# Kernel optimization log

Measured on AMD Instinct MI355X. Metric: run time of the kernel, lower is better.

The kernel has to match this reference:

```python
import jax, jax.numpy as jnp
import numpy as np

DT = 0.1  # discretization step (matches init kwarg dt)


def setup_inputs() -> dict:
    key = jax.random.key(0)
    k1, k2, k3, k4 = jax.random.split(key, 4)
    Bsz, L, D, N = 16, 4096, 128, 64
    x = jax.random.normal(k1, (Bsz, L, D), dtype=jnp.float32)
    # torch uses torch.rand for A; shift by -N*I so A is Hurwitz and the
    # 4096-step recurrence stays numerically stable (same math, stable init).
    A = jax.random.uniform(k2, (D, N, N), dtype=jnp.float32) - float(N) * jnp.eye(N, dtype=jnp.float32)
    B = jax.random.uniform(k3, (D, N, 1), dtype=jnp.float32)
    C = jax.random.uniform(k4, (D, 1, N), dtype=jnp.float32)
    return {"x": x, "A": A, "B": B, "C": C}


def _discretize(A, B):
    # Bilinear (Tustin) transform, per channel d: [D, N, N]
    N = A.shape[-1]
    I = jnp.eye(N, dtype=A.dtype)[None, :, :]
    inv = jnp.linalg.inv(I - A * (DT / 2))
    A_bar = inv @ (I + A * (DT / 2))          # [D, N, N]
    B_bar = (inv @ B) * DT                    # [D, N, 1]
    return A_bar, B_bar


def reference(x, A, B, C):
    # x: [Bsz, L, D]; A: [D, N, N]; B: [D, N, 1]; C: [D, 1, N]
    Bsz, L, D = x.shape
    N = A.shape[-1]
    A_bar, B_bar = _discretize(A, B)
    Bb = B_bar[:, :, 0]                       # [D, N]
    Cv = C[:, 0, :]                           # [D, N]
    xs = jnp.moveaxis(x, 1, 0)                # [L, Bsz, D]
    h0 = jnp.zeros((Bsz, D, N), dtype=x.dtype)

    def step(h, x_t):
        # h_new[b,d,m] = sum_n A_bar[d,m,n] h[b,d,n] + x_t[b,d] * Bb[d,m]
        h = jnp.einsum('dmn,bdn->bdm', A_bar, h) + x_t[:, :, None] * Bb[None]
        y_t = jnp.einsum('bdn,dn->bd', h, Cv)
        return h, y_t

    _, ys = jax.lax.scan(step, h0, xs)        # ys: [L, Bsz, D]
    return jnp.moveaxis(ys, 0, 1)             # [Bsz, L, D]
```

## Files before the change

kernel.cpp:

```cpp
#include <hip/hip_runtime.h>

typedef float f4 __attribute__((ext_vector_type(4)));

#define PAD 68

#define SEED_C2 0.0251681f
#define SEED_C1 (-0.262380f)
#define SEED_C0 0.895613f

__device__ __forceinline__ void mm_acc(const float* L, const float* R,
                                       int i0, int j0, float acc[16]) {
  #pragma unroll
  for (int m = 0; m < 16; ++m) acc[m] = 0.f;
  #pragma unroll
  for (int n = 0; n < 64; n += 4) {
    f4 La[4], Rb[4];
    #pragma unroll
    for (int m = 0; m < 4; ++m) La[m] = *(const f4*)&L[(i0 + m) * PAD + n];
    #pragma unroll
    for (int p = 0; p < 4; ++p) Rb[p] = *(const f4*)&R[(n + p) * PAD + j0];
    #pragma unroll
    for (int m = 0; m < 4; ++m)
      #pragma unroll
      for (int p = 0; p < 4; ++p)
        #pragma unroll
        for (int c = 0; c < 4; ++c)
          acc[m * 4 + c] += La[m][p] * Rb[p][c];
  }
}

__device__ __forceinline__ void store_tile(float* Dst, int i0, int j0, const float acc[16]) {
  #pragma unroll
  for (int m = 0; m < 4; ++m) {
    f4 t = {acc[m*4+0], acc[m*4+1], acc[m*4+2], acc[m*4+3]};
    *(f4*)&Dst[(i0 + m) * PAD + j0] = t;
  }
}

__global__ __launch_bounds__(256) void s4_discretize(
    const float* __restrict__ Ag,
    const float* __restrict__ Bg,
    const float* __restrict__ Cg,
    float* __restrict__ Kout)
{
  __shared__ float Ms[64 * PAD];
  __shared__ float Xs[64 * PAD];
  __shared__ float Ts[64 * PAD];
  __shared__ float C4[4][65];
  __shared__ float U8[64][8];
  __shared__ float Bv[64], Cv0[64], Bb[64];
  __shared__ float Pr[4][64];

  const int d   = blockIdx.x;
  const int tid = threadIdx.x;
  const int i0  = (tid >> 4) << 2;
  const int j0  = (tid & 15) << 2;
  const int q   = tid >> 6;
  const int ln  = tid & 63;

  for (int idx = tid; idx < 4096; idx += 256) {
    int i = idx >> 6, j = idx & 63;
    float a = Ag[(size_t)d * 4096 + idx];
    Ms[i * PAD + j] = ((i == j) ? 1.f : 0.f) - 0.05f * a;
  }
  if (tid < 64) { Bv[tid] = Bg[d * 64 + tid]; Cv0[tid] = Cg[d * 64 + tid]; }
  __syncthreads();

  float acc[16];

  mm_acc(Ms, Ms, i0, j0, acc);
  store_tile(Ts, i0, j0, acc);
  __syncthreads();

  for (int idx = tid; idx < 4096; idx += 256) {
    int i = idx >> 6, j = idx & 63;
    Xs[i * PAD + j] = SEED_C2 * Ts[i * PAD + j] + SEED_C1 * Ms[i * PAD + j]
                    + ((i == j) ? SEED_C0 : 0.f);
  }
  __syncthreads();

  mm_acc(Ms, Xs, i0, j0, acc);
  store_tile(Ts, i0, j0, acc);
  __syncthreads();
  mm_acc(Xs, Ts, i0, j0, acc);
  __syncthreads();
  #pragma unroll
  for (int m = 0; m < 4; ++m) {
    f4 xo = *(const f4*)&Xs[(i0 + m) * PAD + j0];
    f4 t = {acc[m*4+0], acc[m*4+1], acc[m*4+2], acc[m*4+3]};
    *(f4*)&Xs[(i0 + m) * PAD + j0] = 2.f * xo - t;
  }
  __syncthreads();

  {
    float p = 0.f;
    #pragma unroll
    for (int m = 0; m < 16; ++m) p += Xs[ln * PAD + q * 16 + m] * Bv[q * 16 + m];
    Pr[q][ln] = p;
  }
  for (int idx = tid; idx < 4096; idx += 256) {
    int i = idx >> 6, j = idx & 63;
    Ms[i * PAD + j] = 2.f * Xs[i * PAD + j] - ((i == j) ? 1.f : 0.f);
  }
  __syncthreads();
  if (tid < 64) Bb[tid] = 0.1f * (Pr[0][tid] + Pr[1][tid] + Pr[2][tid] + Pr[3][tid]);
  __syncthreads();

  if (tid < 64) C4[0][tid] = Cv0[tid];
  __syncthreads();
  for (int j = 1; j < 4; ++j) {
    float p = 0.f;
    #pragma unroll
    for (int m = 0; m < 16; ++m) p += C4[j - 1][q * 16 + m] * Ms[(q * 16 + m) * PAD + ln];
    Pr[q][ln] = p;
    __syncthreads();
    if (q == 0) C4[j][ln] = Pr[0][ln] + Pr[1][ln] + Pr[2][ln] + Pr[3][ln];
    __syncthreads();
  }

  mm_acc(Ms, Ms, i0, j0, acc);
  #pragma unroll
  for (int m = 0; m < 4; ++m) {
    f4 t = {acc[m*4+0], acc[m*4+1], acc[m*4+2], acc[m*4+3]};
    *(f4*)&Ts[(i0 + m) * PAD + j0] = t;
  }
  __syncthreads();
  mm_acc(Ts, Ts, i0, j0, acc);
  __syncthreads();
  #pragma unroll
  for (int m = 0; m < 4; ++m) {
    f4 t = {acc[m*4+0], acc[m*4+1], acc[m*4+2], acc[m*4+3]};
    *(f4*)&Xs[(i0 + m) * PAD + j0] = t;
  }
  __syncthreads();

  if (tid < 64) U8[tid][0] = Bb[tid];
  __syncthreads();
  for (int i = 1; i < 8; ++i) {
    float p = 0.f;
    #pragma unroll
    for (int m = 0; m < 16; ++m) p += Xs[ln * PAD + q * 16 + m] * U8[q * 16 + m][i - 1];
    Pr[q][ln] = p;
    __syncthreads();
    if (q == 0) U8[ln][i] = Pr[0][ln] + Pr[1][ln] + Pr[2][ln] + Pr[3][ln];
    __syncthreads();
  }

  if (tid < 32) {
    int i = tid >> 2, j = tid & 3;
    float s = 0.f;
    #pragma unroll
    for (int n = 0; n < 64; ++n) s += C4[j][n] * U8[n][i];
    Kout[tid * 128 + d] = s;
  }
}

__global__ __launch_bounds__(256, 4) void s4_conv(
    const float* __restrict__ xg,
    const float* __restrict__ Ktg,
    float* __restrict__ yg)
{
  __shared__ float xs[287 * 32];
  __shared__ float Ks[32 * 32];

  const int tid = threadIdx.y * 32 + threadIdx.x;
  const int tc  = blockIdx.x;
  const int dq  = blockIdx.y;
  const int b   = blockIdx.z;
  const int d0  = dq * 32;
  const int t0  = tc * 256;

  for (int idx = tid; idx < 1024; idx += 256)
    Ks[idx] = Ktg[(idx >> 5) * 128 + d0 + (idx & 31)];

  const float* xb = xg + (size_t)b * 4096 * 128 + d0;
  for (int idx = tid; idx < 287 * 8; idx += 256) {
    int row = idx >> 3, c4 = (idx & 7) << 2;
    int t = t0 - 31 + row;
    f4 v = {0.f, 0.f, 0.f, 0.f};
    if (t >= 0) v = *(const f4*)&xb[(size_t)t * 128 + c4];
    *(f4*)&xs[row * 32 + c4] = v;
  }
  __syncthreads();

  const int dl = threadIdx.x;
  const int g  = threadIdx.y;

  float acc[32];
  #pragma unroll
  for (int t = 0; t < 32; ++t) acc[t] = 0.f;

  float w[47];
  #pragma unroll
  for (int k0 = 0; k0 < 32; k0 += 16) {
    const int base = g * 32 + 16 - k0;
    #pragma unroll
    for (int jj = 0; jj < 47; ++jj) w[jj] = xs[(base + jj) * 32 + dl];
    #pragma unroll
    for (int k = k0; k < k0 + 16; ++k) {
      float kv = Ks[k * 32 + dl];
      #pragma unroll
      for (int t = 0; t < 32; ++t)
        acc[t] += kv * w[t + (k0 + 15 - k)];
    }
  }

  float* yb = yg + ((size_t)b * 4096 + t0 + g * 32) * 128 + d0 + dl;
  #pragma unroll
  for (int t = 0; t < 32; ++t)
    yb[(size_t)t * 128] = acc[t];
}

extern "C" void kernel_launch(void* const* d_in, const int* in_sizes, int n_in,
                              void* d_out, int out_size, void* d_ws, size_t ws_size,
                              hipStream_t stream) {
  const float* x = (const float*)d_in[0];
  const float* A = (const float*)d_in[1];
  const float* B = (const float*)d_in[2];
  const float* C = (const float*)d_in[3];
  float* y  = (float*)d_out;
  float* Kt = (float*)d_ws;

  s4_discretize<<<128, 256, 0, stream>>>(A, B, C, Kt);
  dim3 grid(16, 4, 16), block(32, 8);
  s4_conv<<<grid, block, 0, stream>>>(x, Kt, y);
}
```

Before: 109.8 us.

## Restructure discretize kernel: fewer matmuls, 8x4 tiles, shuffle reductions

Reworks the per-channel discretization kernel. The seed computation is fused into the first matmul epilogue, and the Newton step now writes (2I - M·X) directly. The A_bar^4 squaring matmul is replaced by 15 sequential matrix-vector products with A_bar^2, combined with C and C·A_bar to form the 32 kernel taps. Matmuls use 8x4 register tiles on 128 threads, and the partial-sum reductions go through shared memory plus warp shuffles instead of a separate reduction pass. This cuts matmul count and barriers, but half the threads sit idle during matmuls and the matvec chain is longer; the conv kernel, which likely dominates runtime, is unchanged.

```diff
diff --git a/kernel.cpp b/kernel.cpp
--- a/kernel.cpp
+++ b/kernel.cpp
@@ -8,32 +8,24 @@
 #define SEED_C1 (-0.262380f)
 #define SEED_C0 0.895613f
 
-__device__ __forceinline__ void mm_acc(const float* L, const float* R,
-                                       int i0, int j0, float acc[16]) {
-  #pragma unroll
-  for (int m = 0; m < 16; ++m) acc[m] = 0.f;
+__device__ __forceinline__ void mm_acc8x4(const float* L, const float* R,
+                                          int i0, int j0, float acc[32]) {
+  #pragma unroll
+  for (int m = 0; m < 32; ++m) acc[m] = 0.f;
   #pragma unroll
   for (int n = 0; n < 64; n += 4) {
-    f4 La[4], Rb[4];
-    #pragma unroll
-    for (int m = 0; m < 4; ++m) La[m] = *(const f4*)&L[(i0 + m) * PAD + n];
+    f4 La[8], Rb[4];
+    #pragma unroll
+    for (int m = 0; m < 8; ++m) La[m] = *(const f4*)&L[(i0 + m) * PAD + n];
     #pragma unroll
     for (int p = 0; p < 4; ++p) Rb[p] = *(const f4*)&R[(n + p) * PAD + j0];
     #pragma unroll
-    for (int m = 0; m < 4; ++m)
+    for (int m = 0; m < 8; ++m)
       #pragma unroll
       for (int p = 0; p < 4; ++p)
         #pragma unroll
         for (int c = 0; c < 4; ++c)
           acc[m * 4 + c] += La[m][p] * Rb[p][c];
-  }
-}
-
-__device__ __forceinline__ void store_tile(float* Dst, int i0, int j0, const float acc[16]) {
-  #pragma unroll
-  for (int m = 0; m < 4; ++m) {
-    f4 t = {acc[m*4+0], acc[m*4+1], acc[m*4+2], acc[m*4+3]};
-    *(f4*)&Dst[(i0 + m) * PAD + j0] = t;
   }
 }
 
@@ -46,17 +38,18 @@
   __shared__ float Ms[64 * PAD];
   __shared__ float Xs[64 * PAD];
   __shared__ float Ts[64 * PAD];
-  __shared__ float C4[4][65];
-  __shared__ float U8[64][8];
-  __shared__ float Bv[64], Cv0[64], Bb[64];
+  __shared__ float U16[16][PAD];
   __shared__ float Pr[4][64];
+  __shared__ float Bv[64], Cv0[64], Bb[64], Cc1[64];
 
   const int d   = blockIdx.x;
   const int tid = threadIdx.x;
-  const int i0  = (tid >> 4) << 2;
+  const int i0  = (tid >> 4) << 3;
   const int j0  = (tid & 15) << 2;
   const int q   = tid >> 6;
   const int ln  = tid & 63;
+  const int co  = tid >> 2;
+  const int cc  = tid & 3;
 
   for (int idx = tid; idx < 4096; idx += 256) {
     int i = idx >> 6, j = idx & 63;
@@ -66,29 +59,44 @@
   if (tid < 64) { Bv[tid] = Bg[d * 64 + tid]; Cv0[tid] = Cg[d * 64 + tid]; }
   __syncthreads();
 
-  float acc[16];
-
-  mm_acc(Ms, Ms, i0, j0, acc);
-  store_tile(Ts, i0, j0, acc);
-  __syncthreads();
-
-  for (int idx = tid; idx < 4096; idx += 256) {
-    int i = idx >> 6, j = idx & 63;
-    Xs[i * PAD + j] = SEED_C2 * Ts[i * PAD + j] + SEED_C1 * Ms[i * PAD + j]
-                    + ((i == j) ? SEED_C0 : 0.f);
-  }
-  __syncthreads();
-
-  mm_acc(Ms, Xs, i0, j0, acc);
-  store_tile(Ts, i0, j0, acc);
-  __syncthreads();
-  mm_acc(Xs, Ts, i0, j0, acc);
-  __syncthreads();
-  #pragma unroll
-  for (int m = 0; m < 4; ++m) {
-    f4 xo = *(const f4*)&Xs[(i0 + m) * PAD + j0];
-    f4 t = {acc[m*4+0], acc[m*4+1], acc[m*4+2], acc[m*4+3]};
-    *(f4*)&Xs[(i0 + m) * PAD + j0] = 2.f * xo - t;
+  float acc[32];
+
+  if (tid < 128) {
+    mm_acc8x4(Ms, Ms, i0, j0, acc);
+    #pragma unroll
+    for (int m = 0; m < 8; ++m) {
+      f4 mo = *(const f4*)&Ms[(i0 + m) * PAD + j0];
+      f4 t;
+      #pragma unroll
+      for (int c = 0; c < 4; ++c)
+        t[c] = SEED_C2 * acc[m*4+c] + SEED_C1 * mo[c]
+             + ((i0 + m == j0 + c) ? SEED_C0 : 0.f);
+      *(f4*)&Xs[(i0 + m) * PAD + j0] = t;
+    }
+  }
+  __syncthreads();
+
+  if (tid < 128) {
+    mm_acc8x4(Ms, Xs, i0, j0, acc);
+    #pragma unroll
+    for (int m = 0; m < 8; ++m) {
+      f4 t;
+      #pragma unroll
+      for (int c = 0; c < 4; ++c)
+        t[c] = ((i0 + m == j0 + c) ? 2.f : 0.f) - acc[m*4+c];
+      *(f4*)&Ts[(i0 + m) * PAD + j0] = t;
+    }
+  }
+  __syncthreads();
+
+  if (tid < 128) mm_acc8x4(Xs, Ts, i0, j0, acc);
+  __syncthreads();
+  if (tid < 128) {
+    #pragma unroll
+    for (int m = 0; m < 8; ++m) {
+      f4 t = {acc[m*4+0], acc[m*4+1], acc[m*4+2], acc[m*4+3]};
+      *(f4*)&Xs[(i0 + m) * PAD + j0] = t;
+    }
   }
   __syncthreads();
 
@@ -106,52 +114,53 @@
   if (tid < 64) Bb[tid] = 0.1f * (Pr[0][tid] + Pr[1][tid] + Pr[2][tid] + Pr[3][tid]);
   __syncthreads();
 
-  if (tid < 64) C4[0][tid] = Cv0[tid];
-  __syncthreads();
-  for (int j = 1; j < 4; ++j) {
-    float p = 0.f;
-    #pragma unroll
-    for (int m = 0; m < 16; ++m) p += C4[j - 1][q * 16 + m] * Ms[(q * 16 + m) * PAD + ln];
-    Pr[q][ln] = p;
+  {
+    float p = 0.f;
+    #pragma unroll
+    for (int m = 0; m < 16; ++m)
+      p += Cv0[cc * 16 + m] * Ms[(cc * 16 + m) * PAD + co];
+    p += __shfl_xor(p, 1);
+    p += __shfl_xor(p, 2);
+    if (cc == 0) Cc1[co] = p;
+  }
+  if (tid < 128) {
+    mm_acc8x4(Ms, Ms, i0, j0, acc);
+    #pragma unroll
+    for (int m = 0; m < 8; ++m) {
+      f4 t = {acc[m*4+0], acc[m*4+1], acc[m*4+2], acc[m*4+3]};
+      *(f4*)&Ts[(i0 + m) * PAD + j0] = t;
+    }
+  }
+  if (tid < 64) U16[0][tid] = Bb[tid];
+  __syncthreads();
+
+  for (int i = 1; i < 16; ++i) {
+    const float* Arow = &Ts[co * PAD + cc * 16];
+    const float* uv   = &U16[i - 1][cc * 16];
+    float p = 0.f;
+    #pragma unroll
+    for (int j = 0; j < 4; ++j) {
+      f4 a = *(const f4*)&Arow[4 * j];
+      f4 u = *(const f4*)&uv[4 * j];
+      p += a[0]*u[0] + a[1]*u[1] + a[2]*u[2] + a[3]*u[3];
+    }
+    p += __shfl_xor(p, 1);
+    p += __shfl_xor(p, 2);
+    if (cc == 0) U16[i][co] = p;
     __syncthreads();
-    if (q == 0) C4[j][ln] = Pr[0][ln] + Pr[1][ln] + Pr[2][ln] + Pr[3][ln];
-    __syncthreads();
-  }
-
-  mm_acc(Ms, Ms, i0, j0, acc);
-  #pragma unroll
-  for (int m = 0; m < 4; ++m) {
-    f4 t = {acc[m*4+0], acc[m*4+1], acc[m*4+2], acc[m*4+3]};
-    *(f4*)&Ts[(i0 + m) * PAD + j0] = t;
-  }
-  __syncthreads();
-  mm_acc(Ts, Ts, i0, j0, acc);
-  __syncthreads();
-  #pragma unroll
-  for (int m = 0; m < 4; ++m) {
-    f4 t = {acc[m*4+0], acc[m*4+1], acc[m*4+2], acc[m*4+3]};
-    *(f4*)&Xs[(i0 + m) * PAD + j0] = t;
-  }
-  __syncthreads();
-
-  if (tid < 64) U8[tid][0] = Bb[tid];
-  __syncthreads();
-  for (int i = 1; i < 8; ++i) {
-    float p = 0.f;
-    #pragma unroll
-    for (int m = 0; m < 16; ++m) p += Xs[ln * PAD + q * 16 + m] * U8[q * 16 + m][i - 1];
-    Pr[q][ln] = p;
-    __syncthreads();
-    if (q == 0) U8[ln][i] = Pr[0][ln] + Pr[1][ln] + Pr[2][ln] + Pr[3][ln];
-    __syncthreads();
-  }
-
-  if (tid < 32) {
-    int i = tid >> 2, j = tid & 3;
-    float s = 0.f;
-    #pragma unroll
-    for (int n = 0; n < 64; ++n) s += C4[j][n] * U8[n][i];
-    Kout[tid * 128 + d] = s;
+  }
+
+  {
+    const int k = tid >> 3, e = tid & 7;
+    const float* cvec = (k & 1) ? Cc1 : Cv0;
+    const float* uvec = U16[k >> 1];
+    float p = 0.f;
+    #pragma unroll
+    for (int j = 0; j < 8; ++j) p += cvec[e * 8 + j] * uvec[e * 8 + j];
+    p += __shfl_xor(p, 1);
+    p += __shfl_xor(p, 2);
+    p += __shfl_xor(p, 4);
+    if (e == 0) Kout[k * 128 + d] = p;
   }
 }
 
```

New measurement: 115.0 us. +4.8%, slower.
